# Performance work log

Measured on AMD Instinct MI355X. Metric: run time of the kernel, lower is better.

The kernel has to match this reference:

```python
import jax, jax.numpy as jnp
import numpy as np

L = 2048   # query length (== type_weights rows)
S = 2048   # key/value length
E = 1024   # embed_dim
H = 16     # num_heads
D = E // H # head_dim
LN_EPS = 1e-5


def setup_inputs() -> dict:
    key = jax.random.key(0)
    ks = jax.random.split(key, 16)
    n = lambda k, shape, s=1.0: jax.random.normal(k, shape, dtype=jnp.float32) * s
    return {
        "query": n(ks[0], (L, 1, E)),
        "key": n(ks[1], (S, 1, E)),
        "value": n(ks[2], (S, 1, E)),
        "type_weights": jax.random.uniform(ks[3], (L, 2), dtype=jnp.float32),
        "time_emb": n(ks[4], (S, E)),
        # learned parameters
        "in_proj_w": n(ks[5], (3 * E, E), 0.02),
        "in_proj_b": jnp.zeros((3 * E,), jnp.float32),
        "out_proj_w": n(ks[6], (E, E), 0.02),
        "out_proj_b": jnp.zeros((E,), jnp.float32),
        "time_proj_w": n(ks[7], (H, E), 0.02),
        "time_proj_b": jnp.zeros((H,), jnp.float32),
        "type_bias_w": n(ks[8], (H, 2), 0.02),
        "type_bias_b": jnp.zeros((H,), jnp.float32),
        "ln_w": jnp.ones((E,), jnp.float32),
        "ln_b": jnp.zeros((E,), jnp.float32),
    }


def reference(query, key, value, type_weights, time_emb,
              in_proj_w, in_proj_b, out_proj_w, out_proj_b,
              time_proj_w, time_proj_b, type_bias_w, type_bias_b,
              ln_w, ln_b):
    q = query[:, 0, :]   # [L,E]
    k = key[:, 0, :]     # [S,E]
    v = value[:, 0, :]   # [S,E]

    wq, wk, wv = jnp.split(in_proj_w, 3, axis=0)
    bq, bk, bv = jnp.split(in_proj_b, 3)
    qp = (q @ wq.T + bq).reshape(L, H, D)
    kp = (k @ wk.T + bk).reshape(S, H, D)
    vp = (v @ wv.T + bv).reshape(S, H, D)

    scale = 1.0 / np.sqrt(D)
    scores = jnp.einsum('lhd,shd->hls', qp, kp) * scale  # [H,L,S]

    # additive type bias: per (head, query position), constant over S
    qbias = type_weights @ type_bias_w.T + type_bias_b   # [L,H]
    scores = scores + qbias.T[:, :, None]                # broadcast over S

    # NOTE: the original computes a time bias from time_emb via time_proj but
    # never uses it; output is independent of time_emb/time_proj.

    attn = jax.nn.softmax(scores, axis=-1)               # [H,L,S]
    ctx = jnp.einsum('hls,shd->lhd', attn, vp).reshape(L, E)
    out = ctx @ out_proj_w.T + out_proj_b                # [L,E]

    res = q + out
    mu = jnp.mean(res, axis=-1, keepdims=True)
    var = jnp.var(res, axis=-1, keepdims=True)
    y = (res - mu) / jnp.sqrt(var + LN_EPS) * ln_w + ln_b
    return y[:, None, :]  # [L,1,E]
```

## Files before the change

kernel.cpp:

```cpp
#include <hip/hip_runtime.h>
#include <hip/hip_bf16.h>
#include <cstdint>

#define L_DIM 2048
#define S_DIM 2048
#define E_DIM 1024
#define H_DIM 16
#define D_DIM 64
#define NSPLIT 4
#define SCHUNK (S_DIM / NSPLIT)

typedef __attribute__((ext_vector_type(4))) short short4v;
typedef __attribute__((ext_vector_type(8))) short short8v;
typedef __attribute__((ext_vector_type(4))) float f32x4;

__device__ __forceinline__ short f2bf(float f) {
  union { float f; uint32_t u; } v; v.f = f;
  uint32_t r = (v.u + 0x7fffu + ((v.u >> 16) & 1u)) >> 16;
  return (short)(r & 0xffffu);
}
__device__ __forceinline__ float bf2f(short s) {
  union { uint32_t u; float f; } v; v.u = ((uint32_t)(uint16_t)s) << 16;
  return v.f;
}
__device__ __forceinline__ short f2bf_hw(float f) {
  __hip_bfloat16 h = __float2bfloat16(f);
  return __builtin_bit_cast(short, h);
}

__global__ __launch_bounds__(256) void convert_all(
    const float* __restrict__ q, const float* __restrict__ k,
    const float* __restrict__ v, const float* __restrict__ win,
    const float* __restrict__ wout, short* __restrict__ dst)
{
  const int64_t i = (int64_t)blockIdx.x * 256 + threadIdx.x;
  const int64_t NQ = (int64_t)L_DIM * E_DIM / 4;
  const int64_t NW = (int64_t)3 * E_DIM * E_DIM / 4;
  const float* src; int64_t off;
  if (i < NQ)               { src = q;    off = i; }
  else if (i < 2 * NQ)      { src = k;    off = i - NQ; }
  else if (i < 3 * NQ)      { src = v;    off = i - 2 * NQ; }
  else if (i < 3 * NQ + NW) { src = win;  off = i - 3 * NQ; }
  else                      { src = wout; off = i - (3 * NQ + NW); }
  const float4 val = ((const float4*)src)[off];
  short4v o;
  o.x = f2bf(val.x); o.y = f2bf(val.y); o.z = f2bf(val.z); o.w = f2bf(val.w);
  ((short4v*)dst)[i] = o;
}

__device__ __forceinline__ void gemm_stage(
    const short* __restrict__ A, const short* __restrict__ B,
    const int K, const int m0, const int n0, const int kt,
    short* As, short* Bs, const int t, const int w)
{
#pragma unroll
  for (int j = 0; j < 4; ++j) {
    const int ci = j * 256 + t;
    const int r  = ci >> 3;
    const int cs = (ci & 7) ^ (r & 7);
    const int64_t goff = (int64_t)r * K + kt * 64 + cs * 8;
    const int lbase = (j * 256 + w * 64) * 8;
    __builtin_amdgcn_global_load_lds(
        (const __attribute__((address_space(1))) void*)(A + (int64_t)m0 * K + goff),
        (__attribute__((address_space(3))) void*)(As + lbase), 16, 0, 0);
    __builtin_amdgcn_global_load_lds(
        (const __attribute__((address_space(1))) void*)(B + (int64_t)n0 * K + goff),
        (__attribute__((address_space(3))) void*)(Bs + lbase), 16, 0, 0);
  }
}

__device__ __forceinline__ void gemm128_core(
    const short* __restrict__ A, const short* __restrict__ B,
    const int K, const int m0, const int n0,
    short* lds, f32x4 acc[4][4])
{
  const int t = threadIdx.x;
  const int lane = t & 63;
  const int w = t >> 6;
  const int wr = w >> 1, wc = w & 1;
  const int lr = lane & 15, g = lane >> 4;
  short* As0 = lds;
  short* Bs0 = lds + 8192;
  short* As1 = lds + 16384;
  short* Bs1 = lds + 24576;

#pragma unroll
  for (int i = 0; i < 4; ++i)
#pragma unroll
    for (int j = 0; j < 4; ++j)
      acc[i][j] = (f32x4){0.f, 0.f, 0.f, 0.f};

  const int nkt = K >> 6;
  gemm_stage(A, B, K, m0, n0, 0, As0, Bs0, t, w);
  __syncthreads();

  for (int kt = 0; kt < nkt; ++kt) {
    short* As = (kt & 1) ? As1 : As0;
    short* Bs = (kt & 1) ? Bs1 : Bs0;
    short* An = (kt & 1) ? As0 : As1;
    short* Bn = (kt & 1) ? Bs0 : Bs1;
    if (kt + 1 < nkt)
      gemm_stage(A, B, K, m0, n0, kt + 1, An, Bn, t, w);

#pragma unroll
    for (int kk = 0; kk < 2; ++kk) {
      short8v af[4], bfr[4];
#pragma unroll
      for (int mt = 0; mt < 4; ++mt) {
        const int r  = wr * 64 + mt * 16 + lr;
        const int ch = (kk * 4 + g) ^ (r & 7);
        af[mt] = *(const short8v*)(As + r * 64 + ch * 8);
      }
#pragma unroll
      for (int nt = 0; nt < 4; ++nt) {
        const int r  = wc * 64 + nt * 16 + lr;
        const int ch = (kk * 4 + g) ^ (r & 7);
        bfr[nt] = *(const short8v*)(Bs + r * 64 + ch * 8);
      }
#pragma unroll
      for (int mt = 0; mt < 4; ++mt)
#pragma unroll
        for (int nt = 0; nt < 4; ++nt)
          acc[mt][nt] = __builtin_amdgcn_mfma_f32_16x16x32_bf16(
              af[mt], bfr[nt], acc[mt][nt], 0, 0, 0);
    }
    __syncthreads();
  }
}

__global__ __launch_bounds__(256) void proj_gemm(
    const short* __restrict__ qkv_bf, const short* __restrict__ win_bf,
    const float* __restrict__ in_b,
    short* __restrict__ qp, short* __restrict__ kp, short* __restrict__ vpT)
{
  __shared__ short lds[128 * 64 * 4];
  const int z  = blockIdx.z;
  const int m0 = blockIdx.y * 128;
  const int n0 = blockIdx.x * 128;
  const short* A = qkv_bf + (int64_t)z * L_DIM * E_DIM;
  const short* B = win_bf + (int64_t)z * E_DIM * E_DIM;
  const float* bias = in_b + z * E_DIM;
  f32x4 acc[4][4];
  gemm128_core(A, B, E_DIM, m0, n0, lds, acc);

  const int lane = threadIdx.x & 63;
  const int w = threadIdx.x >> 6;
  const int wr = w >> 1, wc = w & 1;
  const int lr = lane & 15, g = lane >> 4;

  if (z == 2) {
#pragma unroll
    for (int nt = 0; nt < 4; ++nt) {
      const int col = n0 + wc * 64 + nt * 16 + lr;
      const float bv = bias[col];
#pragma unroll
      for (int mt = 0; mt < 4; ++mt) {
        const int row = m0 + wr * 64 + mt * 16 + g * 4;
        short4v o;
#pragma unroll
        for (int i = 0; i < 4; ++i) o[i] = f2bf(acc[mt][nt][i] + bv);
        *(short4v*)(vpT + (int64_t)col * S_DIM + row) = o;
      }
    }
  } else {
    short* outp = (z == 0) ? qp : kp;
    const float qscale = (z == 0) ? 0.18033688011112042f : 1.0f;
#pragma unroll
    for (int nt = 0; nt < 4; ++nt) {
      const int col = n0 + wc * 64 + nt * 16 + lr;
      const float bv = bias[col];
#pragma unroll
      for (int mt = 0; mt < 4; ++mt) {
        const int row = m0 + wr * 64 + mt * 16 + g * 4;
#pragma unroll
        for (int i = 0; i < 4; ++i)
          outp[(int64_t)(row + i) * E_DIM + col] = f2bf((acc[mt][nt][i] + bv) * qscale);
      }
    }
  }
}

__global__ __launch_bounds__(256) void outproj_gemm(
    const short* __restrict__ ctx, const short* __restrict__ wout_bf,
    const float* __restrict__ out_b, const float* __restrict__ resid,
    float* __restrict__ res)
{
  __shared__ short lds[128 * 64 * 4];
  const int m0 = blockIdx.y * 128;
  const int n0 = blockIdx.x * 128;
  f32x4 acc[4][4];
  gemm128_core(ctx, wout_bf, E_DIM, m0, n0, lds, acc);

  const int lane = threadIdx.x & 63;
  const int w = threadIdx.x >> 6;
  const int wr = w >> 1, wc = w & 1;
  const int lr = lane & 15, g = lane >> 4;
#pragma unroll
  for (int nt = 0; nt < 4; ++nt) {
    const int col = n0 + wc * 64 + nt * 16 + lr;
    const float bv = out_b[col];
#pragma unroll
    for (int mt = 0; mt < 4; ++mt) {
      const int row = m0 + wr * 64 + mt * 16 + g * 4;
#pragma unroll
      for (int i = 0; i < 4; ++i)
        res[(int64_t)(row + i) * E_DIM + col] =
            acc[mt][nt][i] + bv + resid[(int64_t)(row + i) * E_DIM + col];
    }
  }
}

__device__ __forceinline__ void attn_stage(
    const short* __restrict__ kp, const short* __restrict__ vpT,
    int h, int sbase, short* Ks, short* Vs, int t, int w)
{
#pragma unroll
  for (int j = 0; j < 2; ++j) {
    const int ci = j * 256 + t;
    const int r  = ci >> 3;
    const int cs = (ci & 7) ^ (r & 7);
    const int lbase = (j * 256 + w * 64) * 8;
    __builtin_amdgcn_global_load_lds(
        (const __attribute__((address_space(1))) void*)
            (kp + (int64_t)(sbase + r) * E_DIM + h * D_DIM + cs * 8),
        (__attribute__((address_space(3))) void*)(Ks + lbase), 16, 0, 0);
    __builtin_amdgcn_global_load_lds(
        (const __attribute__((address_space(1))) void*)
            (vpT + (int64_t)(h * D_DIM + r) * S_DIM + sbase + cs * 8),
        (__attribute__((address_space(3))) void*)(Vs + lbase), 16, 0, 0);
  }
}

__global__ __launch_bounds__(256, 4) void attn_kernel(
    const short* __restrict__ qp, const short* __restrict__ kp,
    const short* __restrict__ vpT, short* __restrict__ part,
    float* __restrict__ stats)
{
  __shared__ short lds[64 * 64 * 4];
  short* Ks0 = lds;
  short* Vs0 = lds + 4096;
  short* Ks1 = lds + 8192;
  short* Vs1 = lds + 12288;

  const int t = threadIdx.x;
  const int lane = t & 63;
  const int w = t >> 6;
  const int lr = lane & 15, g = lane >> 4;
  const int bid0 = blockIdx.x;
  const int bid = (bid0 & 7) * 128 + (bid0 >> 3);
  const int lt = bid & 15;
  const int h  = (bid >> 4) & 15;
  const int z  = bid >> 8;
  const int l0 = lt * 128 + w * 32;

  const short* q0 = qp + (int64_t)(l0 + lr) * E_DIM + h * D_DIM + g * 8;
  const short8v qa00 = *(const short8v*)q0;
  const short8v qa01 = *(const short8v*)(q0 + 32);
  const short8v qa10 = *(const short8v*)(q0 + 16 * E_DIM);
  const short8v qa11 = *(const short8v*)(q0 + 16 * E_DIM + 32);

  f32x4 acc0[4], acc1[4];
#pragma unroll
  for (int b = 0; b < 4; ++b) {
    acc0[b] = (f32x4){0.f, 0.f, 0.f, 0.f};
    acc1[b] = (f32x4){0.f, 0.f, 0.f, 0.f};
  }
  float ls0 = 0.f, ls1 = 0.f;
  const float BMAX = 8.0f;

  const int sbeg = z * SCHUNK;
  const int NT = SCHUNK / 64;

  attn_stage(kp, vpT, h, sbeg, Ks0, Vs0, t, w);
  __syncthreads();

  for (int stp = 0; stp < NT; ++stp) {
    short* Ks = (stp & 1) ? Ks1 : Ks0;
    short* Vs = (stp & 1) ? Vs1 : Vs0;
    short* Kn = (stp & 1) ? Ks0 : Ks1;
    short* Vn = (stp & 1) ? Vs0 : Vs1;
    if (stp + 1 < NT)
      attn_stage(kp, vpT, h, sbeg + (stp + 1) * 64, Kn, Vn, t, w);

#pragma unroll
    for (int kk = 0; kk < 4; ++kk) {
      const int rK = kk * 16 + lr;
      const short8v ka0 = *(const short8v*)(Ks + rK * 64 + ((g    ) ^ (rK & 7)) * 8);
      const short8v ka1 = *(const short8v*)(Ks + rK * 64 + ((g + 4) ^ (rK & 7)) * 8);
      short4v vv[4];
#pragma unroll
      for (int b = 0; b < 4; ++b) {
        const int rV = b * 16 + lr;
        const int cc = kk * 2 + (g >> 1);
        vv[b] = *(const short4v*)(Vs + rV * 64 + (cc ^ (rV & 7)) * 8 + (g & 1) * 4);
      }

      f32x4 st0 = (f32x4){0.f, 0.f, 0.f, 0.f};
      f32x4 st1 = (f32x4){0.f, 0.f, 0.f, 0.f};
      st0 = __builtin_amdgcn_mfma_f32_16x16x32_bf16(ka0, qa00, st0, 0, 0, 0);
      st0 = __builtin_amdgcn_mfma_f32_16x16x32_bf16(ka1, qa01, st0, 0, 0, 0);
      st1 = __builtin_amdgcn_mfma_f32_16x16x32_bf16(ka0, qa10, st1, 0, 0, 0);
      st1 = __builtin_amdgcn_mfma_f32_16x16x32_bf16(ka1, qa11, st1, 0, 0, 0);

      {
        const float p0 = __builtin_amdgcn_exp2f(st0[0] - BMAX);
        const float p1 = __builtin_amdgcn_exp2f(st0[1] - BMAX);
        const float p2 = __builtin_amdgcn_exp2f(st0[2] - BMAX);
        const float p3 = __builtin_amdgcn_exp2f(st0[3] - BMAX);
        ls0 += (p0 + p1) + (p2 + p3);
        short4v pb;
        pb.x = f2bf_hw(p0); pb.y = f2bf_hw(p1);
        pb.z = f2bf_hw(p2); pb.w = f2bf_hw(p3);
        acc0[0] = __builtin_amdgcn_mfma_f32_16x16x16bf16_1k(vv[0], pb, acc0[0], 0, 0, 0);
        acc0[1] = __builtin_amdgcn_mfma_f32_16x16x16bf16_1k(vv[1], pb, acc0[1], 0, 0, 0);
        acc0[2] = __builtin_amdgcn_mfma_f32_16x16x16bf16_1k(vv[2], pb, acc0[2], 0, 0, 0);
        acc0[3] = __builtin_amdgcn_mfma_f32_16x16x16bf16_1k(vv[3], pb, acc0[3], 0, 0, 0);
      }
      {
        const float p0 = __builtin_amdgcn_exp2f(st1[0] - BMAX);
        const float p1 = __builtin_amdgcn_exp2f(st1[1] - BMAX);
        const float p2 = __builtin_amdgcn_exp2f(st1[2] - BMAX);
        const float p3 = __builtin_amdgcn_exp2f(st1[3] - BMAX);
        ls1 += (p0 + p1) + (p2 + p3);
        short4v pb;
        pb.x = f2bf_hw(p0); pb.y = f2bf_hw(p1);
        pb.z = f2bf_hw(p2); pb.w = f2bf_hw(p3);
        acc1[0] = __builtin_amdgcn_mfma_f32_16x16x16bf16_1k(vv[0], pb, acc1[0], 0, 0, 0);
        acc1[1] = __builtin_amdgcn_mfma_f32_16x16x16bf16_1k(vv[1], pb, acc1[1], 0, 0, 0);
        acc1[2] = __builtin_amdgcn_mfma_f32_16x16x16bf16_1k(vv[2], pb, acc1[2], 0, 0, 0);
        acc1[3] = __builtin_amdgcn_mfma_f32_16x16x16bf16_1k(vv[3], pb, acc1[3], 0, 0, 0);
      }
    }
    __syncthreads();
  }

  ls0 += __shfl_xor(ls0, 16);
  ls0 += __shfl_xor(ls0, 32);
  ls1 += __shfl_xor(ls1, 16);
  ls1 += __shfl_xor(ls1, 32);

  {
    const int row = l0 + lr;
    short* prow = part + (int64_t)z * (L_DIM * E_DIM)
                       + (int64_t)row * E_DIM + h * D_DIM + g * 4;
#pragma unroll
    for (int b = 0; b < 4; ++b) {
      short4v o;
      o.x = f2bf(acc0[b][0]); o.y = f2bf(acc0[b][1]);
      o.z = f2bf(acc0[b][2]); o.w = f2bf(acc0[b][3]);
      *(short4v*)(prow + b * 16) = o;
    }
    if (g == 0) {
      float2 sv; sv.x = BMAX; sv.y = ls0;
      ((float2*)stats)[(z << 15) + row * H_DIM + h] = sv;
    }
  }
  {
    const int row = l0 + 16 + lr;
    short* prow = part + (int64_t)z * (L_DIM * E_DIM)
                       + (int64_t)row * E_DIM + h * D_DIM + g * 4;
#pragma unroll
    for (int b = 0; b < 4; ++b) {
      short4v o;
      o.x = f2bf(acc1[b][0]); o.y = f2bf(acc1[b][1]);
      o.z = f2bf(acc1[b][2]); o.w = f2bf(acc1[b][3]);
      *(short4v*)(prow + b * 16) = o;
    }
    if (g == 0) {
      float2 sv; sv.x = BMAX; sv.y = ls1;
      ((float2*)stats)[(z << 15) + row * H_DIM + h] = sv;
    }
  }
}

__global__ __launch_bounds__(256) void attn_combine(
    const short* __restrict__ part, const float* __restrict__ stats,
    short* __restrict__ ctx)
{
  const int gid = blockIdx.x * 256 + threadIdx.x;
  const int rh = gid >> 4;
  const int dq = (gid & 15) * 4;
  const int l = rh >> 4, h = rh & 15;
  const int64_t eoff = (int64_t)l * E_DIM + h * D_DIM + dq;
  float o0 = 0.f, o1 = 0.f, o2 = 0.f, o3 = 0.f, Lt = 0.f;
#pragma unroll
  for (int zz = 0; zz < NSPLIT; ++zz) {
    const float2 sv = ((const float2*)stats)[(zz << 15) + rh];
    Lt += sv.y;
    const short4v pv = *(const short4v*)(part + (int64_t)zz * (L_DIM * E_DIM) + eoff);
    o0 += bf2f(pv.x); o1 += bf2f(pv.y);
    o2 += bf2f(pv.z); o3 += bf2f(pv.w);
  }
  const float r = 1.0f / Lt;
  short4v o;
  o.x = f2bf(o0 * r); o.y = f2bf(o1 * r); o.z = f2bf(o2 * r); o.w = f2bf(o3 * r);
  *(short4v*)(ctx + eoff) = o;
}

__global__ __launch_bounds__(256) void ln_kernel(
    const float* __restrict__ res, const float* __restrict__ lnw,
    const float* __restrict__ lnb, float* __restrict__ out)
{
  const int row = blockIdx.x;
  const int t = threadIdx.x;
  const float4 v = ((const float4*)(res + (int64_t)row * E_DIM))[t];
  float s  = v.x + v.y + v.z + v.w;
  float s2 = v.x * v.x + v.y * v.y + v.z * v.z + v.w * v.w;
#pragma unroll
  for (int off = 32; off >= 1; off >>= 1) {
    s  += __shfl_xor(s, off);
    s2 += __shfl_xor(s2, off);
  }
  __shared__ float red[8];
  const int w = t >> 6;
  if ((t & 63) == 0) { red[w] = s; red[4 + w] = s2; }
  __syncthreads();
  const float S  = red[0] + red[1] + red[2] + red[3];
  const float S2 = red[4] + red[5] + red[6] + red[7];
  const float mu = S * (1.0f / E_DIM);
  const float rstd = rsqrtf(S2 * (1.0f / E_DIM) - mu * mu + 1e-5f);
  const float4 wv = ((const float4*)lnw)[t];
  const float4 bv = ((const float4*)lnb)[t];
  float4 o;
  o.x = (v.x - mu) * rstd * wv.x + bv.x;
  o.y = (v.y - mu) * rstd * wv.y + bv.y;
  o.z = (v.z - mu) * rstd * wv.z + bv.z;
  o.w = (v.w - mu) * rstd * wv.w + bv.w;
  ((float4*)(out + (int64_t)row * E_DIM))[t] = o;
}

extern "C" void kernel_launch(void* const* d_in, const int* in_sizes, int n_in,
                              void* d_out, int out_size, void* d_ws, size_t ws_size,
                              hipStream_t stream)
{
  const float* q     = (const float*)d_in[0];
  const float* k     = (const float*)d_in[1];
  const float* v     = (const float*)d_in[2];
  const float* winw  = (const float*)d_in[5];
  const float* winb  = (const float*)d_in[6];
  const float* woutw = (const float*)d_in[7];
  const float* woutb = (const float*)d_in[8];
  const float* lnw   = (const float*)d_in[13];
  const float* lnb   = (const float*)d_in[14];

  short* ws = (short*)d_ws;
  const int64_t LE = (int64_t)L_DIM * E_DIM;
  const int64_t EE = (int64_t)E_DIM * E_DIM;
  short* qkv_bf  = ws;
  short* win_bf  = ws + 3 * LE;
  short* wout_bf = win_bf + 3 * EE;
  short* qp      = wout_bf + EE;
  short* kp      = qp + LE;
  short* vpT     = kp + LE;
  short* ctx     = vpT + LE;
  float* res     = (float*)(ctx + LE);

  short* part  = ws;
  float* stats = (float*)(ws + (int64_t)NSPLIT * LE);

  convert_all<<<10240, 256, 0, stream>>>(q, k, v, winw, woutw, qkv_bf);
  proj_gemm<<<dim3(8, 16, 3), 256, 0, stream>>>(qkv_bf, win_bf, winb, qp, kp, vpT);
  attn_kernel<<<dim3(1024), 256, 0, stream>>>(qp, kp, vpT, part, stats);
  attn_combine<<<2048, 256, 0, stream>>>(part, stats, ctx);
  outproj_gemm<<<dim3(8, 16), 256, 0, stream>>>(ctx, wout_bf, woutb, q, res);
  ln_kernel<<<L_DIM, 256, 0, stream>>>(res, lnw, lnb, (float*)d_out);
}
```

Baseline: 89.99 us.

## Use 8 waves of 16 query rows each in attention kernel

The attention block grows from 4 to 8 wavefronts (512 threads), and each wave now handles 16 query rows instead of 32. The K/V tile staging is split across all 512 threads with one load per thread instead of two. The aim is more waves in flight and fewer registers per wave to hide latency. In exchange, each wave gets less reuse of the K/V tile fragments it reads from LDS, so LDS traffic per MFMA rises. The launch bound of 8 blocks per CU may also be impossible to reach given LDS use.

```diff
diff --git a/kernel.cpp b/kernel.cpp
--- a/kernel.cpp
+++ b/kernel.cpp
@@ -214,24 +214,20 @@
     const short* __restrict__ kp, const short* __restrict__ vpT,
     int h, int sbase, short* Ks, short* Vs, int t, int w)
 {
-#pragma unroll
-  for (int j = 0; j < 2; ++j) {
-    const int ci = j * 256 + t;
-    const int r  = ci >> 3;
-    const int cs = (ci & 7) ^ (r & 7);
-    const int lbase = (j * 256 + w * 64) * 8;
-    __builtin_amdgcn_global_load_lds(
-        (const __attribute__((address_space(1))) void*)
-            (kp + (int64_t)(sbase + r) * E_DIM + h * D_DIM + cs * 8),
-        (__attribute__((address_space(3))) void*)(Ks + lbase), 16, 0, 0);
-    __builtin_amdgcn_global_load_lds(
-        (const __attribute__((address_space(1))) void*)
-            (vpT + (int64_t)(h * D_DIM + r) * S_DIM + sbase + cs * 8),
-        (__attribute__((address_space(3))) void*)(Vs + lbase), 16, 0, 0);
-  }
-}
-
-__global__ __launch_bounds__(256, 4) void attn_kernel(
+  const int r  = t >> 3;
+  const int cs = (t & 7) ^ (r & 7);
+  const int lbase = (w * 64) * 8;
+  __builtin_amdgcn_global_load_lds(
+      (const __attribute__((address_space(1))) void*)
+          (kp + (int64_t)(sbase + r) * E_DIM + h * D_DIM + cs * 8),
+      (__attribute__((address_space(3))) void*)(Ks + lbase), 16, 0, 0);
+  __builtin_amdgcn_global_load_lds(
+      (const __attribute__((address_space(1))) void*)
+          (vpT + (int64_t)(h * D_DIM + r) * S_DIM + sbase + cs * 8),
+      (__attribute__((address_space(3))) void*)(Vs + lbase), 16, 0, 0);
+}
+
+__global__ __launch_bounds__(512, 8) void attn_kernel(
     const short* __restrict__ qp, const short* __restrict__ kp,
     const short* __restrict__ vpT, short* __restrict__ part,
     float* __restrict__ stats)
@@ -251,21 +247,16 @@
   const int lt = bid & 15;
   const int h  = (bid >> 4) & 15;
   const int z  = bid >> 8;
-  const int l0 = lt * 128 + w * 32;
+  const int l0 = lt * 128 + w * 16;
 
   const short* q0 = qp + (int64_t)(l0 + lr) * E_DIM + h * D_DIM + g * 8;
-  const short8v qa00 = *(const short8v*)q0;
-  const short8v qa01 = *(const short8v*)(q0 + 32);
-  const short8v qa10 = *(const short8v*)(q0 + 16 * E_DIM);
-  const short8v qa11 = *(const short8v*)(q0 + 16 * E_DIM + 32);
-
-  f32x4 acc0[4], acc1[4];
-#pragma unroll
-  for (int b = 0; b < 4; ++b) {
-    acc0[b] = (f32x4){0.f, 0.f, 0.f, 0.f};
-    acc1[b] = (f32x4){0.f, 0.f, 0.f, 0.f};
-  }
-  float ls0 = 0.f, ls1 = 0.f;
+  const short8v qa0 = *(const short8v*)q0;
+  const short8v qa1 = *(const short8v*)(q0 + 32);
+
+  f32x4 acc[4];
+#pragma unroll
+  for (int b = 0; b < 4; ++b) acc[b] = (f32x4){0.f, 0.f, 0.f, 0.f};
+  float ls = 0.f;
   const float BMAX = 8.0f;
 
   const int sbeg = z * SCHUNK;
@@ -295,81 +286,42 @@
         vv[b] = *(const short4v*)(Vs + rV * 64 + (cc ^ (rV & 7)) * 8 + (g & 1) * 4);
       }
 
-      f32x4 st0 = (f32x4){0.f, 0.f, 0.f, 0.f};
-      f32x4 st1 = (f32x4){0.f, 0.f, 0.f, 0.f};
-      st0 = __builtin_amdgcn_mfma_f32_16x16x32_bf16(ka0, qa00, st0, 0, 0, 0);
-      st0 = __builtin_amdgcn_mfma_f32_16x16x32_bf16(ka1, qa01, st0, 0, 0, 0);
-      st1 = __builtin_amdgcn_mfma_f32_16x16x32_bf16(ka0, qa10, st1, 0, 0, 0);
-      st1 = __builtin_amdgcn_mfma_f32_16x16x32_bf16(ka1, qa11, st1, 0, 0, 0);
-
-      {
-        const float p0 = __builtin_amdgcn_exp2f(st0[0] - BMAX);
-        const float p1 = __builtin_amdgcn_exp2f(st0[1] - BMAX);
-        const float p2 = __builtin_amdgcn_exp2f(st0[2] - BMAX);
-        const float p3 = __builtin_amdgcn_exp2f(st0[3] - BMAX);
-        ls0 += (p0 + p1) + (p2 + p3);
-        short4v pb;
-        pb.x = f2bf_hw(p0); pb.y = f2bf_hw(p1);
-        pb.z = f2bf_hw(p2); pb.w = f2bf_hw(p3);
-        acc0[0] = __builtin_amdgcn_mfma_f32_16x16x16bf16_1k(vv[0], pb, acc0[0], 0, 0, 0);
-        acc0[1] = __builtin_amdgcn_mfma_f32_16x16x16bf16_1k(vv[1], pb, acc0[1], 0, 0, 0);
-        acc0[2] = __builtin_amdgcn_mfma_f32_16x16x16bf16_1k(vv[2], pb, acc0[2], 0, 0, 0);
-        acc0[3] = __builtin_amdgcn_mfma_f32_16x16x16bf16_1k(vv[3], pb, acc0[3], 0, 0, 0);
-      }
-      {
-        const float p0 = __builtin_amdgcn_exp2f(st1[0] - BMAX);
-        const float p1 = __builtin_amdgcn_exp2f(st1[1] - BMAX);
-        const float p2 = __builtin_amdgcn_exp2f(st1[2] - BMAX);
-        const float p3 = __builtin_amdgcn_exp2f(st1[3] - BMAX);
-        ls1 += (p0 + p1) + (p2 + p3);
-        short4v pb;
-        pb.x = f2bf_hw(p0); pb.y = f2bf_hw(p1);
-        pb.z = f2bf_hw(p2); pb.w = f2bf_hw(p3);
-        acc1[0] = __builtin_amdgcn_mfma_f32_16x16x16bf16_1k(vv[0], pb, acc1[0], 0, 0, 0);
-        acc1[1] = __builtin_amdgcn_mfma_f32_16x16x16bf16_1k(vv[1], pb, acc1[1], 0, 0, 0);
-        acc1[2] = __builtin_amdgcn_mfma_f32_16x16x16bf16_1k(vv[2], pb, acc1[2], 0, 0, 0);
-        acc1[3] = __builtin_amdgcn_mfma_f32_16x16x16bf16_1k(vv[3], pb, acc1[3], 0, 0, 0);
-      }
+      f32x4 st = (f32x4){0.f, 0.f, 0.f, 0.f};
+      st = __builtin_amdgcn_mfma_f32_16x16x32_bf16(ka0, qa0, st, 0, 0, 0);
+      st = __builtin_amdgcn_mfma_f32_16x16x32_bf16(ka1, qa1, st, 0, 0, 0);
+
+      const float p0 = __builtin_amdgcn_exp2f(st[0] - BMAX);
+      const float p1 = __builtin_amdgcn_exp2f(st[1] - BMAX);
+      const float p2 = __builtin_amdgcn_exp2f(st[2] - BMAX);
+      const float p3 = __builtin_amdgcn_exp2f(st[3] - BMAX);
+      ls += (p0 + p1) + (p2 + p3);
+      short4v pb;
+      pb.x = f2bf_hw(p0); pb.y = f2bf_hw(p1);
+      pb.z = f2bf_hw(p2); pb.w = f2bf_hw(p3);
+      acc[0] = __builtin_amdgcn_mfma_f32_16x16x16bf16_1k(vv[0], pb, acc[0], 0, 0, 0);
+      acc[1] = __builtin_amdgcn_mfma_f32_16x16x16bf16_1k(vv[1], pb, acc[1], 0, 0, 0);
+      acc[2] = __builtin_amdgcn_mfma_f32_16x16x16bf16_1k(vv[2], pb, acc[2], 0, 0, 0);
+      acc[3] = __builtin_amdgcn_mfma_f32_16x16x16bf16_1k(vv[3], pb, acc[3], 0, 0, 0);
     }
     __syncthreads();
   }
 
-  ls0 += __shfl_xor(ls0, 16);
-  ls0 += __shfl_xor(ls0, 32);
-  ls1 += __shfl_xor(ls1, 16);
-  ls1 += __shfl_xor(ls1, 32);
-
-  {
-    const int row = l0 + lr;
-    short* prow = part + (int64_t)z * (L_DIM * E_DIM)
-                       + (int64_t)row * E_DIM + h * D_DIM + g * 4;
-#pragma unroll
-    for (int b = 0; b < 4; ++b) {
-      short4v o;
-      o.x = f2bf(acc0[b][0]); o.y = f2bf(acc0[b][1]);
-      o.z = f2bf(acc0[b][2]); o.w = f2bf(acc0[b][3]);
-      *(short4v*)(prow + b * 16) = o;
-    }
-    if (g == 0) {
-      float2 sv; sv.x = BMAX; sv.y = ls0;
-      ((float2*)stats)[(z << 15) + row * H_DIM + h] = sv;
-    }
-  }
-  {
-    const int row = l0 + 16 + lr;
-    short* prow = part + (int64_t)z * (L_DIM * E_DIM)
-                       + (int64_t)row * E_DIM + h * D_DIM + g * 4;
-#pragma unroll
-    for (int b = 0; b < 4; ++b) {
-      short4v o;
-      o.x = f2bf(acc1[b][0]); o.y = f2bf(acc1[b][1]);
-      o.z = f2bf(acc1[b][2]); o.w = f2bf(acc1[b][3]);
-      *(short4v*)(prow + b * 16) = o;
-    }
-    if (g == 0) {
-      float2 sv; sv.x = BMAX; sv.y = ls1;
-      ((float2*)stats)[(z << 15) + row * H_DIM + h] = sv;
-    }
+  ls += __shfl_xor(ls, 16);
+  ls += __shfl_xor(ls, 32);
+
+  const int row = l0 + lr;
+  short* prow = part + (int64_t)z * (L_DIM * E_DIM)
+                     + (int64_t)row * E_DIM + h * D_DIM + g * 4;
+#pragma unroll
+  for (int b = 0; b < 4; ++b) {
+    short4v o;
+    o.x = f2bf(acc[b][0]); o.y = f2bf(acc[b][1]);
+    o.z = f2bf(acc[b][2]); o.w = f2bf(acc[b][3]);
+    *(short4v*)(prow + b * 16) = o;
+  }
+  if (g == 0) {
+    float2 sv; sv.x = BMAX; sv.y = ls;
+    ((float2*)stats)[(z << 15) + row * H_DIM + h] = sv;
   }
 }
 
@@ -460,7 +412,7 @@
 
   convert_all<<<10240, 256, 0, stream>>>(q, k, v, winw, woutw, qkv_bf);
   proj_gemm<<<dim3(8, 16, 3), 256, 0, stream>>>(qkv_bf, win_bf, winb, qp, kp, vpT);
-  attn_kernel<<<dim3(1024), 256, 0, stream>>>(qp, kp, vpT, part, stats);
+  attn_kernel<<<dim3(1024), 512, 0, stream>>>(qp, kp, vpT, part, stats);
   attn_combine<<<2048, 256, 0, stream>>>(part, stats, ctx);
   outproj_gemm<<<dim3(8, 16), 256, 0, stream>>>(ctx, wout_bf, woutb, q, res);
   ln_kernel<<<L_DIM, 256, 0, stream>>>(res, lnw, lnb, (float*)d_out);
```

Result: no change. 91.45 us (+1.6%).
